# Kernel tuning notes

Measured on AMD Instinct MI355X. Metric: run time of the kernel, lower is better.

## Reference

```python
import jax, jax.numpy as jnp
from jax import lax
import numpy as np

DIM = 1024
HID = 1536
K = 4
C_CONST = 8.0


def setup_inputs() -> dict:
    key = jax.random.key(0)
    ks = jax.random.split(key, 12)
    d, h = DIM, HID
    x = jax.random.normal(ks[0], (4, 4096, d), dtype=jnp.float32)
    Wg = jax.random.normal(ks[1], (h, d), dtype=jnp.float32) * d ** -0.5
    Wi = jax.random.normal(ks[2], (h, d), dtype=jnp.float32) * d ** -0.5
    conv_w = jax.random.normal(ks[3], (h, 1, K), dtype=jnp.float32) * (1.0 / K) ** 0.5
    conv_b = jax.random.normal(ks[4], (h,), dtype=jnp.float32) * 0.02
    lru_Wi = jax.random.normal(ks[5], (h, h), dtype=jnp.float32) * h ** -0.5
    lru_bi = jnp.zeros((h,), dtype=jnp.float32)
    lru_Wg = jax.random.normal(ks[6], (h, h), dtype=jnp.float32) * h ** -0.5
    lru_bg = jnp.zeros((h,), dtype=jnp.float32)
    lam = jnp.linspace(-4.323, -9.0, h, dtype=jnp.float32)
    Wo = jax.random.normal(ks[7], (d, h), dtype=jnp.float32) * h ** -0.5
    return {"x": x, "Wg": Wg, "Wi": Wi, "conv_w": conv_w, "conv_b": conv_b,
            "lru_Wi": lru_Wi, "lru_bi": lru_bi, "lru_Wg": lru_Wg, "lru_bg": lru_bg,
            "lam": lam, "Wo": Wo}


def _hawk_forward(x, Wg, Wi, conv_w, conv_b, lru_Wi, lru_bi, lru_Wg, lru_bg, lam, Wo):
    H = Wg.shape[0]
    k = conv_w.shape[-1]
    gate = jnp.einsum('bsd,hd->bsh', x, Wg)        # [B,S,H]
    u = jnp.einsum('bsd,hd->bsh', x, Wi)           # [B,S,H]
    # causal depthwise conv1d (torch pads k-1 both sides then slices [:S] == left-pad k-1)
    y = lax.conv_general_dilated(
        u.transpose(0, 2, 1), conv_w, window_strides=(1,),
        padding=[(k - 1, 0)], dimension_numbers=('NCH', 'OIH', 'NCH'),
        feature_group_count=H) + conv_b[None, :, None]
    y = y.transpose(0, 2, 1)                        # [B,S,H]
    # RG_LRU
    ig = jax.nn.sigmoid(jnp.einsum('bsh,gh->bsg', y, lru_Wi) + lru_bi)
    rg = jax.nn.sigmoid(jnp.einsum('bsh,gh->bsg', y, lru_Wg) + lru_bg)
    alpha = jnp.exp(-C_CONST * jax.nn.softplus(lam) * rg)
    beta = jnp.sqrt(1.0 - alpha ** 2 + 1e-6)
    xbeta = beta * ig * y
    # diagonal linear recurrence h_t = alpha_t * h_{t-1} + xbeta_t via associative scan
    def combine(c1, c2):
        a1, b1 = c1
        a2, b2 = c2
        return a1 * a2, a2 * b1 + b2
    _, h = lax.associative_scan(combine, (alpha, xbeta), axis=1)
    return jnp.einsum('bsh,dh->bsd', jax.nn.gelu(gate, approximate=False) * h, Wo)


def reference(x, Wg, Wi, conv_w, conv_b, lru_Wi, lru_bi, lru_Wg, lru_bg, lam, Wo):
    return _hawk_forward(x, Wg, Wi, conv_w, conv_b, lru_Wi, lru_bi, lru_Wg, lru_bg, lam, Wo)
```

## Files before the change

### kernel.cpp

```cpp
#include <hip/hip_runtime.h>
#include <hip/hip_bf16.h>
#include <math.h>

#define B_  4
#define S_  4096
#define D_  1024
#define H_  1536
#define M_  (B_*S_)
#define CCONST 8.0f

#define CL  128
#define NC  (S_/CL)

#define BM 128
#define BN 128
#define BK 32

using bf16x8 = __attribute__((ext_vector_type(8))) short;
using f32x4  = __attribute__((ext_vector_type(4))) float;
using u16x8  = __attribute__((ext_vector_type(8))) unsigned short;

__device__ __forceinline__ float bf2f(unsigned short u){
    union{unsigned i; float f;} v; v.i = ((unsigned)u)<<16; return v.f;
}
__device__ __forceinline__ unsigned short f2bf(float f){
    union{float f; unsigned i;} v; v.f = f;
    unsigned r = v.i + 0x7fffu + ((v.i>>16)&1u);
    return (unsigned short)(r>>16);
}

#define GLOAD16(gp, lp) __builtin_amdgcn_global_load_lds( \
    (const __attribute__((address_space(1))) void*)(gp),  \
    (__attribute__((address_space(3))) void*)(lp), 16, 0, 0)

__global__ void cast_bf16_kernel(const float* __restrict__ in,
                                 unsigned short* __restrict__ out, int n8)
{
    int i = blockIdx.x*blockDim.x + threadIdx.x;
    if (i >= n8) return;
    const float4* p = reinterpret_cast<const float4*>(in + (size_t)i*8);
    float4 a = p[0], b = p[1];
    u16x8 o;
    o[0]=f2bf(a.x); o[1]=f2bf(a.y); o[2]=f2bf(a.z); o[3]=f2bf(a.w);
    o[4]=f2bf(b.x); o[5]=f2bf(b.y); o[6]=f2bf(b.z); o[7]=f2bf(b.w);
    *reinterpret_cast<u16x8*>(out + (size_t)i*8) = o;
}

template<int MODE>
__global__ __launch_bounds__(256) void gemm_bt(
    const unsigned short* __restrict__ A, const unsigned short* __restrict__ Bw,
    void* __restrict__ out, int M, int N, int K)
{
    __shared__ alignas(16) unsigned short As[BM*BK];
    __shared__ alignas(16) unsigned short Bs[BN*BK];
    const int tid = threadIdx.x, lane = tid&63, wid = tid>>6;
    const int row0 = blockIdx.x*BM, col0 = blockIdx.y*BN;
    const int wr = (wid>>1)*64, wc = (wid&1)*64;
    const int lr = lane&15, kg = lane>>4;

    f32x4 acc[4][4];
    #pragma unroll
    for (int m=0;m<4;m++)
        #pragma unroll
        for (int n=0;n<4;n++) acc[m][n] = (f32x4){0.f,0.f,0.f,0.f};

    for (int k0=0;k0<K;k0+=BK){
        #pragma unroll
        for (int r=0;r<2;r++){
            int eb = (r*256 + wid*64)*8;
            int le = eb + lane*8;
            int arow = le>>5, acol = le&31;
            GLOAD16(&A [(size_t)(row0+arow)*K + (k0+acol)], &As[eb]);
            GLOAD16(&Bw[(size_t)(col0+arow)*K + (k0+acol)], &Bs[eb]);
        }
        __syncthreads();
        bf16x8 af[4], bfr[4];
        #pragma unroll
        for (int m=0;m<4;m++) af[m]  = *(const bf16x8*)&As[(wr + m*16 + lr)*BK + kg*8];
        #pragma unroll
        for (int n=0;n<4;n++) bfr[n] = *(const bf16x8*)&Bs[(wc + n*16 + lr)*BK + kg*8];
        #pragma unroll
        for (int m=0;m<4;m++)
            #pragma unroll
            for (int n=0;n<4;n++)
                acc[m][n] = __builtin_amdgcn_mfma_f32_16x16x32_bf16(af[m], bfr[n], acc[m][n], 0,0,0);
        __syncthreads();
    }

    #pragma unroll
    for (int n=0;n<4;n++){
        int c = col0 + wc + n*16 + lr;
        #pragma unroll
        for (int m=0;m<4;m++){
            int rbase = row0 + wr + m*16 + kg*4;
            #pragma unroll
            for (int j=0;j<4;j++){
                float v = acc[m][n][j];
                size_t idx = (size_t)(rbase+j)*N + c;
                if constexpr (MODE==0){
                    ((unsigned short*)out)[idx] = f2bf(v);
                } else if constexpr (MODE==1){
                    float g = 0.5f*v*(1.0f + erff(v*0.70710678118654752f));
                    ((unsigned short*)out)[idx] = f2bf(g);
                } else {
                    ((float*)out)[idx] = v;
                }
            }
        }
    }
}

__global__ __launch_bounds__(256) void gemm_dual(
    const unsigned short* __restrict__ Yb,
    const unsigned short* __restrict__ Bi, const unsigned short* __restrict__ Bg,
    const float* __restrict__ bi, const float* __restrict__ bg,
    const float* __restrict__ lam,
    unsigned short* __restrict__ la, unsigned short* __restrict__ xbeta)
{
    const int K = H_, N = H_;
    __shared__ alignas(16) unsigned short As [BM*BK];
    __shared__ alignas(16) unsigned short Bsi[BN*BK];
    __shared__ alignas(16) unsigned short Bsg[BN*BK];
    const int tid = threadIdx.x, lane = tid&63, wid = tid>>6;
    const int row0 = blockIdx.x*BM, col0 = blockIdx.y*BN;
    const int wr = (wid>>1)*64, wc = (wid&1)*64;
    const int lr = lane&15, kg = lane>>4;

    f32x4 ai[4][4], ag[4][4];
    #pragma unroll
    for (int m=0;m<4;m++)
        #pragma unroll
        for (int n=0;n<4;n++){ ai[m][n]=(f32x4){0.f,0.f,0.f,0.f}; ag[m][n]=(f32x4){0.f,0.f,0.f,0.f}; }

    for (int k0=0;k0<K;k0+=BK){
        #pragma unroll
        for (int r=0;r<2;r++){
            int eb = (r*256 + wid*64)*8;
            int le = eb + lane*8;
            int arow = le>>5, acol = le&31;
            GLOAD16(&Yb[(size_t)(row0+arow)*K + (k0+acol)], &As [eb]);
            GLOAD16(&Bi[(size_t)(col0+arow)*K + (k0+acol)], &Bsi[eb]);
            GLOAD16(&Bg[(size_t)(col0+arow)*K + (k0+acol)], &Bsg[eb]);
        }
        __syncthreads();
        bf16x8 af[4], bfi[4], bfg[4];
        #pragma unroll
        for (int m=0;m<4;m++) af[m]  = *(const bf16x8*)&As [(wr + m*16 + lr)*BK + kg*8];
        #pragma unroll
        for (int n=0;n<4;n++){ bfi[n] = *(const bf16x8*)&Bsi[(wc + n*16 + lr)*BK + kg*8];
                               bfg[n] = *(const bf16x8*)&Bsg[(wc + n*16 + lr)*BK + kg*8]; }
        #pragma unroll
        for (int m=0;m<4;m++)
            #pragma unroll
            for (int n=0;n<4;n++){
                ai[m][n] = __builtin_amdgcn_mfma_f32_16x16x32_bf16(af[m], bfi[n], ai[m][n], 0,0,0);
                ag[m][n] = __builtin_amdgcn_mfma_f32_16x16x32_bf16(af[m], bfg[n], ag[m][n], 0,0,0);
            }
        __syncthreads();
    }

    #pragma unroll
    for (int n=0;n<4;n++){
        int c = col0 + wc + n*16 + lr;
        float bic = bi[c], bgc = bg[c];
        float sp = log1pf(expf(lam[c]));
        float msp = -CCONST*sp;
        #pragma unroll
        for (int m=0;m<4;m++){
            int rbase = row0 + wr + m*16 + kg*4;
            #pragma unroll
            for (int j=0;j<4;j++){
                size_t idx = (size_t)(rbase+j)*N + c;
                float zi = ai[m][n][j] + bic;
                float zg = ag[m][n][j] + bgc;
                float ig = 1.f/(1.f+expf(-zi));
                float rg = 1.f/(1.f+expf(-zg));
                float lav = msp*rg;
                float a  = expf(lav);
                float bt = sqrtf(1.f - a*a + 1e-6f);
                float y  = bf2f(Yb[idx]);
                la[idx]    = f2bf(lav);
                xbeta[idx] = f2bf(bt*ig*y);
            }
        }
    }
}

__global__ void conv_kernel(const unsigned short* __restrict__ U,
                            const float* __restrict__ W,
                            const float* __restrict__ Cb,
                            unsigned short* __restrict__ Y)
{
    int gid = blockIdx.x*blockDim.x + threadIdx.x;
    int hc = gid % (H_/8); int m = gid / (H_/8);
    int s = m & (S_-1);
    int h0 = hc*8;
    size_t base = (size_t)m*H_ + h0;
    float acc[8];
    #pragma unroll
    for (int j=0;j<8;j++) acc[j] = Cb[h0+j];
    #pragma unroll
    for (int i=0;i<4;i++){
        int ss = s - 3 + i;
        if (ss < 0) continue;
        u16x8 uv = *reinterpret_cast<const u16x8*>(&U[(size_t)(m-3+i)*H_ + h0]);
        #pragma unroll
        for (int j=0;j<8;j++) acc[j] += W[(h0+j)*4 + i] * bf2f(uv[j]);
    }
    u16x8 o;
    #pragma unroll
    for (int j=0;j<8;j++) o[j] = f2bf(acc[j]);
    *reinterpret_cast<u16x8*>(&Y[base]) = o;
}

__global__ void scan1_kernel(const unsigned short* __restrict__ la,
                             const unsigned short* __restrict__ xbeta,
                             float* __restrict__ Ac, float* __restrict__ Bc)
{
    int h = blockIdx.x*blockDim.x + threadIdx.x;
    int b = blockIdx.y, c = blockIdx.z;
    size_t base = ((size_t)b*S_ + (size_t)c*CL)*H_ + h;
    float sa = 0.f, Bv = 0.f;
    for (int t=0;t<CL;t++){
        float l = bf2f(la   [base + (size_t)t*H_]);
        float x = bf2f(xbeta[base + (size_t)t*H_]);
        Bv = expf(l)*Bv + x;
        sa += l;
    }
    size_t o = ((size_t)c*B_ + b)*H_ + h;
    Ac[o] = expf(sa); Bc[o] = Bv;
}

__global__ void scan2_kernel(const float* __restrict__ Ac, const float* __restrict__ Bc,
                             float* __restrict__ Hin)
{
    int idx = blockIdx.x*blockDim.x + threadIdx.x;
    int b = idx / H_, h = idx % H_;
    float hcur = 0.f;
    for (int c=0;c<NC;c++){
        size_t o = ((size_t)c*B_ + b)*H_ + h;
        Hin[o] = hcur;
        hcur = Ac[o]*hcur + Bc[o];
    }
}

__global__ void scan3_kernel(const unsigned short* __restrict__ la,
                             const unsigned short* __restrict__ xbeta,
                             const float* __restrict__ Hin,
                             const unsigned short* __restrict__ Gg,
                             unsigned short* __restrict__ Vb)
{
    int h = blockIdx.x*blockDim.x + threadIdx.x;
    int b = blockIdx.y, c = blockIdx.z;
    size_t base = ((size_t)b*S_ + (size_t)c*CL)*H_ + h;
    float hcur = Hin[((size_t)c*B_ + b)*H_ + h];
    for (int t=0;t<CL;t++){
        size_t o = base + (size_t)t*H_;
        float l = bf2f(la[o]);
        float x = bf2f(xbeta[o]);
        hcur = expf(l)*hcur + x;
        float g = bf2f(Gg[o]);
        Vb[o] = f2bf(g*hcur);
    }
}

extern "C" void kernel_launch(void* const* d_in, const int* in_sizes, int n_in,
                              void* d_out, int out_size, void* d_ws, size_t ws_size,
                              hipStream_t stream)
{
    const float* x      = (const float*)d_in[0];
    const float* Wg     = (const float*)d_in[1];
    const float* Wi     = (const float*)d_in[2];
    const float* conv_w = (const float*)d_in[3];
    const float* conv_b = (const float*)d_in[4];
    const float* lru_Wi = (const float*)d_in[5];
    const float* lru_bi = (const float*)d_in[6];
    const float* lru_Wg = (const float*)d_in[7];
    const float* lru_bg = (const float*)d_in[8];
    const float* lam    = (const float*)d_in[9];
    const float* Wo     = (const float*)d_in[10];
    float* out = (float*)d_out;

    const size_t BY16 = (size_t)M_*H_*2;
    char* w = (char*)d_ws;
    unsigned short* xb    = (unsigned short*)w;
    unsigned short* la    = (unsigned short*)w;  w += BY16;
    unsigned short* ggb   = (unsigned short*)w;  w += BY16;
    unsigned short* ub    = (unsigned short*)w;  w += BY16;
    unsigned short* xbeta = (unsigned short*)w;  w += BY16;
    unsigned short* wgb   = (unsigned short*)w;  w += (size_t)H_*D_*2;
    unsigned short* wib   = (unsigned short*)w;  w += (size_t)H_*D_*2;
    unsigned short* wliB  = (unsigned short*)w;  w += (size_t)H_*H_*2;
    unsigned short* wlgB  = (unsigned short*)w;  w += (size_t)H_*H_*2;
    unsigned short* wob   = (unsigned short*)w;  w += (size_t)D_*H_*2;
    float* Ac  = (float*)w; w += (size_t)NC*B_*H_*4;
    float* Bc  = (float*)w; w += (size_t)NC*B_*H_*4;
    float* Hin = (float*)w; w += (size_t)NC*B_*H_*4;
    unsigned short* yb = (unsigned short*)d_out;
    unsigned short* vb = ub;

    size_t need = (size_t)(w - (char*)d_ws);
    if (ws_size < need) return;

    cast_bf16_kernel<<<(M_*D_/8)/256,   256, 0, stream>>>(x,      xb,   M_*D_/8);
    cast_bf16_kernel<<<(H_*D_/8)/256,   256, 0, stream>>>(Wg,     wgb,  H_*D_/8);
    cast_bf16_kernel<<<(H_*D_/8)/256,   256, 0, stream>>>(Wi,     wib,  H_*D_/8);
    cast_bf16_kernel<<<(H_*H_/8)/256,   256, 0, stream>>>(lru_Wi, wliB, H_*H_/8);
    cast_bf16_kernel<<<(H_*H_/8)/256,   256, 0, stream>>>(lru_Wg, wlgB, H_*H_/8);
    cast_bf16_kernel<<<(D_*H_/8)/256,   256, 0, stream>>>(Wo,     wob,  D_*H_/8);

    gemm_bt<1><<<dim3(M_/BM, H_/BN), 256, 0, stream>>>(xb, wgb, ggb, M_, H_, D_);
    gemm_bt<0><<<dim3(M_/BM, H_/BN), 256, 0, stream>>>(xb, wib, ub,  M_, H_, D_);

    conv_kernel<<<(M_*(H_/8))/256, 256, 0, stream>>>(ub, conv_w, conv_b, yb);

    gemm_dual<<<dim3(M_/BM, H_/BN), 256, 0, stream>>>(yb, wliB, wlgB, lru_bi, lru_bg, lam, la, xbeta);

    scan1_kernel<<<dim3(H_/256, B_, NC), 256, 0, stream>>>(la, xbeta, Ac, Bc);
    scan2_kernel<<<(B_*H_)/256, 256, 0, stream>>>(Ac, Bc, Hin);
    scan3_kernel<<<dim3(H_/256, B_, NC), 256, 0, stream>>>(la, xbeta, Hin, ggb, vb);

    gemm_bt<2><<<dim3(M_/BM, D_/BN), 256, 0, stream>>>(vb, wob, out, M_, D_, H_);
}
```

Baseline: 1.031 ms.

## Double-buffer GEMM LDS tiles and fuse gate/input projections into dual GEMM

Adds double-buffered shared-memory tiles to both GEMM kernels so the next K-slice's global loads are issued while MFMAs run on the current slice, with one barrier per iteration. The gate and input projections, which both read x, are merged into a single dual-output GEMM launch so the activation tile is loaded once per block, with GELU applied in the epilogue. The cost is doubled LDS use (about 48KB for the dual kernel), which may lower occupancy.

```diff
diff --git a/kernel.cpp b/kernel.cpp
--- a/kernel.cpp
+++ b/kernel.cpp
@@ -51,40 +51,49 @@
     const unsigned short* __restrict__ A, const unsigned short* __restrict__ Bw,
     void* __restrict__ out, int M, int N, int K)
 {
-    __shared__ alignas(16) unsigned short As[BM*BK];
-    __shared__ alignas(16) unsigned short Bs[BN*BK];
+    __shared__ alignas(16) unsigned short As[2][BM*BK];
+    __shared__ alignas(16) unsigned short Bs[2][BN*BK];
     const int tid = threadIdx.x, lane = tid&63, wid = tid>>6;
     const int row0 = blockIdx.x*BM, col0 = blockIdx.y*BN;
     const int wr = (wid>>1)*64, wc = (wid&1)*64;
     const int lr = lane&15, kg = lane>>4;
 
+    const int eb0 = (wid*64)*8,  eb1 = ((256 + wid*64))*8;
+    const int le0 = eb0 + lane*8, le1 = eb1 + lane*8;
+    const int ar0 = le0>>5, ac0 = le0&31;
+    const int ar1 = le1>>5, ac1 = le1&31;
+
+    auto stage = [&](int buf, int k0){
+        GLOAD16(&A [(size_t)(row0+ar0)*K + (k0+ac0)], &As[buf][eb0]);
+        GLOAD16(&Bw[(size_t)(col0+ar0)*K + (k0+ac0)], &Bs[buf][eb0]);
+        GLOAD16(&A [(size_t)(row0+ar1)*K + (k0+ac1)], &As[buf][eb1]);
+        GLOAD16(&Bw[(size_t)(col0+ar1)*K + (k0+ac1)], &Bs[buf][eb1]);
+    };
+
     f32x4 acc[4][4];
     #pragma unroll
     for (int m=0;m<4;m++)
         #pragma unroll
         for (int n=0;n<4;n++) acc[m][n] = (f32x4){0.f,0.f,0.f,0.f};
 
-    for (int k0=0;k0<K;k0+=BK){
-        #pragma unroll
-        for (int r=0;r<2;r++){
-            int eb = (r*256 + wid*64)*8;
-            int le = eb + lane*8;
-            int arow = le>>5, acol = le&31;
-            GLOAD16(&A [(size_t)(row0+arow)*K + (k0+acol)], &As[eb]);
-            GLOAD16(&Bw[(size_t)(col0+arow)*K + (k0+acol)], &Bs[eb]);
-        }
-        __syncthreads();
+    const int nk = K/BK;
+    stage(0, 0);
+    __syncthreads();
+    int cur = 0;
+    for (int t=0; t<nk; ++t){
+        if (t+1 < nk) stage(cur^1, (t+1)*BK);
         bf16x8 af[4], bfr[4];
         #pragma unroll
-        for (int m=0;m<4;m++) af[m]  = *(const bf16x8*)&As[(wr + m*16 + lr)*BK + kg*8];
-        #pragma unroll
-        for (int n=0;n<4;n++) bfr[n] = *(const bf16x8*)&Bs[(wc + n*16 + lr)*BK + kg*8];
+        for (int m=0;m<4;m++) af[m]  = *(const bf16x8*)&As[cur][(wr + m*16 + lr)*BK + kg*8];
+        #pragma unroll
+        for (int n=0;n<4;n++) bfr[n] = *(const bf16x8*)&Bs[cur][(wc + n*16 + lr)*BK + kg*8];
         #pragma unroll
         for (int m=0;m<4;m++)
             #pragma unroll
             for (int n=0;n<4;n++)
                 acc[m][n] = __builtin_amdgcn_mfma_f32_16x16x32_bf16(af[m], bfr[n], acc[m][n], 0,0,0);
         __syncthreads();
+        cur ^= 1;
     }
 
     #pragma unroll
@@ -99,9 +108,6 @@
                 size_t idx = (size_t)(rbase+j)*N + c;
                 if constexpr (MODE==0){
                     ((unsigned short*)out)[idx] = f2bf(v);
-                } else if constexpr (MODE==1){
-                    float g = 0.5f*v*(1.0f + erff(v*0.70710678118654752f));
-                    ((unsigned short*)out)[idx] = f2bf(g);
                 } else {
                     ((float*)out)[idx] = v;
                 }
@@ -110,77 +116,98 @@
     }
 }
 
+template<int EPI>
 __global__ __launch_bounds__(256) void gemm_dual(
-    const unsigned short* __restrict__ Yb,
-    const unsigned short* __restrict__ Bi, const unsigned short* __restrict__ Bg,
+    const unsigned short* __restrict__ Aall,
+    const unsigned short* __restrict__ B1, const unsigned short* __restrict__ B2,
+    unsigned short* __restrict__ O1, unsigned short* __restrict__ O2,
     const float* __restrict__ bi, const float* __restrict__ bg,
     const float* __restrict__ lam,
-    unsigned short* __restrict__ la, unsigned short* __restrict__ xbeta)
-{
-    const int K = H_, N = H_;
-    __shared__ alignas(16) unsigned short As [BM*BK];
-    __shared__ alignas(16) unsigned short Bsi[BN*BK];
-    __shared__ alignas(16) unsigned short Bsg[BN*BK];
+    int N, int K)
+{
+    __shared__ alignas(16) unsigned short As [2][BM*BK];
+    __shared__ alignas(16) unsigned short Bs1[2][BN*BK];
+    __shared__ alignas(16) unsigned short Bs2[2][BN*BK];
     const int tid = threadIdx.x, lane = tid&63, wid = tid>>6;
     const int row0 = blockIdx.x*BM, col0 = blockIdx.y*BN;
     const int wr = (wid>>1)*64, wc = (wid&1)*64;
     const int lr = lane&15, kg = lane>>4;
 
-    f32x4 ai[4][4], ag[4][4];
+    const int eb0 = (wid*64)*8,  eb1 = ((256 + wid*64))*8;
+    const int le0 = eb0 + lane*8, le1 = eb1 + lane*8;
+    const int ar0 = le0>>5, ac0 = le0&31;
+    const int ar1 = le1>>5, ac1 = le1&31;
+
+    auto stage = [&](int buf, int k0){
+        GLOAD16(&Aall[(size_t)(row0+ar0)*K + (k0+ac0)], &As [buf][eb0]);
+        GLOAD16(&B1  [(size_t)(col0+ar0)*K + (k0+ac0)], &Bs1[buf][eb0]);
+        GLOAD16(&B2  [(size_t)(col0+ar0)*K + (k0+ac0)], &Bs2[buf][eb0]);
+        GLOAD16(&Aall[(size_t)(row0+ar1)*K + (k0+ac1)], &As [buf][eb1]);
+        GLOAD16(&B1  [(size_t)(col0+ar1)*K + (k0+ac1)], &Bs1[buf][eb1]);
+        GLOAD16(&B2  [(size_t)(col0+ar1)*K + (k0+ac1)], &Bs2[buf][eb1]);
+    };
+
+    f32x4 a1[4][4], a2[4][4];
     #pragma unroll
     for (int m=0;m<4;m++)
         #pragma unroll
-        for (int n=0;n<4;n++){ ai[m][n]=(f32x4){0.f,0.f,0.f,0.f}; ag[m][n]=(f32x4){0.f,0.f,0.f,0.f}; }
-
-    for (int k0=0;k0<K;k0+=BK){
-        #pragma unroll
-        for (int r=0;r<2;r++){
-            int eb = (r*256 + wid*64)*8;
-            int le = eb + lane*8;
-            int arow = le>>5, acol = le&31;
-            GLOAD16(&Yb[(size_t)(row0+arow)*K + (k0+acol)], &As [eb]);
-            GLOAD16(&Bi[(size_t)(col0+arow)*K + (k0+acol)], &Bsi[eb]);
-            GLOAD16(&Bg[(size_t)(col0+arow)*K + (k0+acol)], &Bsg[eb]);
-        }
-        __syncthreads();
-        bf16x8 af[4], bfi[4], bfg[4];
-        #pragma unroll
-        for (int m=0;m<4;m++) af[m]  = *(const bf16x8*)&As [(wr + m*16 + lr)*BK + kg*8];
-        #pragma unroll
-        for (int n=0;n<4;n++){ bfi[n] = *(const bf16x8*)&Bsi[(wc + n*16 + lr)*BK + kg*8];
-                               bfg[n] = *(const bf16x8*)&Bsg[(wc + n*16 + lr)*BK + kg*8]; }
+        for (int n=0;n<4;n++){ a1[m][n]=(f32x4){0.f,0.f,0.f,0.f}; a2[m][n]=(f32x4){0.f,0.f,0.f,0.f}; }
+
+    const int nk = K/BK;
+    stage(0, 0);
+    __syncthreads();
+    int cur = 0;
+    for (int t=0; t<nk; ++t){
+        if (t+1 < nk) stage(cur^1, (t+1)*BK);
+        bf16x8 af[4], b1f[4], b2f[4];
+        #pragma unroll
+        for (int m=0;m<4;m++) af[m]  = *(const bf16x8*)&As [cur][(wr + m*16 + lr)*BK + kg*8];
+        #pragma unroll
+        for (int n=0;n<4;n++){ b1f[n] = *(const bf16x8*)&Bs1[cur][(wc + n*16 + lr)*BK + kg*8];
+                               b2f[n] = *(const bf16x8*)&Bs2[cur][(wc + n*16 + lr)*BK + kg*8]; }
         #pragma unroll
         for (int m=0;m<4;m++)
             #pragma unroll
             for (int n=0;n<4;n++){
-                ai[m][n] = __builtin_amdgcn_mfma_f32_16x16x32_bf16(af[m], bfi[n], ai[m][n], 0,0,0);
-                ag[m][n] = __builtin_amdgcn_mfma_f32_16x16x32_bf16(af[m], bfg[n], ag[m][n], 0,0,0);
+                a1[m][n] = __builtin_amdgcn_mfma_f32_16x16x32_bf16(af[m], b1f[n], a1[m][n], 0,0,0);
+                a2[m][n] = __builtin_amdgcn_mfma_f32_16x16x32_bf16(af[m], b2f[n], a2[m][n], 0,0,0);
             }
         __syncthreads();
+        cur ^= 1;
     }
 
     #pragma unroll
     for (int n=0;n<4;n++){
         int c = col0 + wc + n*16 + lr;
-        float bic = bi[c], bgc = bg[c];
-        float sp = log1pf(expf(lam[c]));
-        float msp = -CCONST*sp;
+        float bic = 0.f, msp = 0.f, bgc = 0.f;
+        if constexpr (EPI==1){
+            bic = bi[c]; bgc = bg[c];
+            msp = -CCONST * log1pf(expf(lam[c]));
+        }
         #pragma unroll
         for (int m=0;m<4;m++){
             int rbase = row0 + wr + m*16 + kg*4;
             #pragma unroll
             for (int j=0;j<4;j++){
                 size_t idx = (size_t)(rbase+j)*N + c;
-                float zi = ai[m][n][j] + bic;
-                float zg = ag[m][n][j] + bgc;
-                float ig = 1.f/(1.f+expf(-zi));
-                float rg = 1.f/(1.f+expf(-zg));
-                float lav = msp*rg;
-                float a  = expf(lav);
-                float bt = sqrtf(1.f - a*a + 1e-6f);
-                float y  = bf2f(Yb[idx]);
-                la[idx]    = f2bf(lav);
-                xbeta[idx] = f2bf(bt*ig*y);
+                float z1 = a1[m][n][j];
+                float z2 = a2[m][n][j];
+                if constexpr (EPI==0){
+                    float g = 0.5f*z1*(1.0f + erff(z1*0.70710678118654752f));
+                    O1[idx] = f2bf(g);
+                    O2[idx] = f2bf(z2);
+                } else {
+                    float zi = z1 + bic;
+                    float zg = z2 + bgc;
+                    float ig = 1.f/(1.f+expf(-zi));
+                    float rg = 1.f/(1.f+expf(-zg));
+                    float lav = msp*rg;
+                    float a  = expf(lav);
+                    float bt = sqrtf(1.f - a*a + 1e-6f);
+                    float y  = bf2f(Aall[idx]);
+                    O1[idx] = f2bf(lav);
+                    O2[idx] = f2bf(bt*ig*y);
+                }
             }
         }
     }
@@ -309,12 +336,13 @@
     cast_bf16_kernel<<<(H_*H_/8)/256,   256, 0, stream>>>(lru_Wg, wlgB, H_*H_/8);
     cast_bf16_kernel<<<(D_*H_/8)/256,   256, 0, stream>>>(Wo,     wob,  D_*H_/8);
 
-    gemm_bt<1><<<dim3(M_/BM, H_/BN), 256, 0, stream>>>(xb, wgb, ggb, M_, H_, D_);
-    gemm_bt<0><<<dim3(M_/BM, H_/BN), 256, 0, stream>>>(xb, wib, ub,  M_, H_, D_);
+    gemm_dual<0><<<dim3(M_/BM, H_/BN), 256, 0, stream>>>(
+        xb, wgb, wib, ggb, ub, nullptr, nullptr, nullptr, H_, D_);
 
     conv_kernel<<<(M_*(H_/8))/256, 256, 0, stream>>>(ub, conv_w, conv_b, yb);
 
-    gemm_dual<<<dim3(M_/BM, H_/BN), 256, 0, stream>>>(yb, wliB, wlgB, lru_bi, lru_bg, lam, la, xbeta);
+    gemm_dual<1><<<dim3(M_/BM, H_/BN), 256, 0, stream>>>(
+        yb, wliB, wlgB, la, xbeta, lru_bi, lru_bg, lam, H_, H_);
 
     scan1_kernel<<<dim3(H_/256, B_, NC), 256, 0, stream>>>(la, xbeta, Ac, Bc);
     scan2_kernel<<<(B_*H_)/256, 256, 0, stream>>>(Ac, Bc, Hin);
```

Measured after the change: 1.093 ms. 1.06x slower.
